# Kernel tuning notes

Measured on AMD Instinct MI355X. Metric: run time of the kernel, lower is better.

The kernel has to match this reference:

```python
import jax, jax.numpy as jnp
import numpy as np
import math

D_MODEL = 256
PRED_LEN = 256
K = 32
LOW_FREQ = 1


def setup_inputs() -> dict:
    key = jax.random.key(0)
    x = jax.random.normal(key, (8, 1024, D_MODEL), dtype=jnp.float32)
    return {"x": x}


def reference(x):
    """x: (b, t, d) -> reconstructed/extrapolated series (b, t+pred_len, d)."""
    b, t, d = x.shape
    k_ = K  # K < t//2, so the explicit-k branch of the torch module is taken

    x_freq = jnp.fft.rfft(x, axis=1)  # (b, t//2+1, d) complex
    if t % 2 == 0:
        x_freq_high = x_freq[:, LOW_FREQ:-1]  # drop DC..low_freq-1 and Nyquist
    else:
        x_freq_high = x_freq[:, LOW_FREQ:]

    # top-k magnitudes over the frequency axis, independently per (b, d)
    mag = jnp.abs(x_freq_high)                                   # (b, F, d)
    _, idx = jax.lax.top_k(jnp.transpose(mag, (0, 2, 1)), k_)    # (b, d, k)
    idx = jnp.transpose(idx, (0, 2, 1)) + LOW_FREQ               # (b, k, d) into x_freq

    x_freq_topk = jnp.take_along_axis(x_freq, idx, axis=1)       # (b, k, d) complex
    freqs = jnp.fft.rfftfreq(t).astype(x.dtype)                  # (t//2+1,)
    f_topk = freqs[idx]                                          # (b, k, d)

    # append conjugate / negative-frequency pair for a real reconstruction
    x_ext = jnp.concatenate([x_freq_topk, jnp.conj(x_freq_topk)], axis=1)  # (b, 2k, d)
    f_ext = jnp.concatenate([f_topk, -f_topk], axis=1)                     # (b, 2k, d)

    t_val = jnp.arange(t + PRED_LEN, dtype=x.dtype)              # (T,)
    amp = (jnp.abs(x_ext) / t)[:, :, None, :]                    # (b, 2k, 1, d)
    phase = jnp.angle(x_ext)[:, :, None, :]                      # (b, 2k, 1, d)
    arg = (2.0 * math.pi) * f_ext[:, :, None, :] * t_val[None, None, :, None] + phase
    x_time = amp * jnp.cos(arg)                                  # (b, 2k, T, d)
    return jnp.sum(x_time, axis=1)                               # (b, T, d)
```

## Files before the change

kernel.cpp:

```cpp
#include <hip/hip_runtime.h>
#include <math.h>

#define T_LEN 1024
#define PRED_LEN 256
#define OUT_T (T_LEN + PRED_LEN)
#define DM 256
#define KSEL 32
#define RTAU 1e-4f

#define PAD16(i) ((i) + ((i) >> 4))
#define C1024F 0.006135923151542565f

__device__ __constant__ float W16RF[16] = {
    1.0f,  0.92387953f,  0.70710678f,  0.38268343f, 0.0f, -0.38268343f, -0.70710678f, -0.92387953f,
   -1.0f, -0.92387953f, -0.70710678f, -0.38268343f, 0.0f,  0.38268343f,  0.70710678f,  0.92387953f };
__device__ __constant__ float W16IF[16] = {
    0.0f, -0.38268343f, -0.70710678f, -0.92387953f, -1.0f, -0.92387953f, -0.70710678f, -0.38268343f,
    0.0f,  0.38268343f,  0.70710678f,  0.92387953f,  1.0f,  0.92387953f,  0.70710678f,  0.38268343f };

#define C1_ 0.92387953251128675613
#define C2_ 0.70710678118654752440
#define C3_ 0.38268343236508977173
__device__ __constant__ double W16R_[16] = {
    1.0,  C1_,  C2_,  C3_, 0.0, -C3_, -C2_, -C1_,
   -1.0, -C1_, -C2_, -C3_, 0.0,  C3_,  C2_,  C1_ };
__device__ __constant__ double W16I_[16] = {
    0.0, -C3_, -C2_, -C1_, -1.0, -C1_, -C2_, -C3_,
    0.0,  C3_,  C2_,  C1_,  1.0,  C1_,  C2_,  C3_ };

__device__ __forceinline__ float2 zval(const float2* __restrict__ xunp,
                                       const unsigned* __restrict__ selw, int k) {
    if (k == 0 || k == 512) return float2{ 0.f, 0.f };
    const int  fold = (k < 512) ? k : (1024 - k);
    const float sgn = (k < 512) ? 1.0f : -1.0f;
    float2 X0 = xunp[fold];
    float2 X1 = xunp[512 + fold];
    const bool s0 = (selw[fold >> 5]        >> (fold & 31)) & 1u;
    const bool s1 = (selw[16 + (fold >> 5)] >> (fold & 31)) & 1u;
    float x0i = sgn * X0.y;
    float x1i = sgn * X1.y;
    float Zr = (s0 ? X0.x : 0.f) - (s1 ? x1i : 0.f);
    float Zi = (s0 ? x0i : 0.f) + (s1 ? X1.x : 0.f);
    return float2{ Zr, -Zi };
}

__device__ __forceinline__ void fft1024(const float2* __restrict__ xin,
                                        const float2* __restrict__ twF,
                                        int lane, int w, float* ar, float* ai) {
    float Fr[4][4], Fi[4][4];
#pragma unroll
    for (int n1a = 0; n1a < 4; ++n1a) {
        float2 a  = xin[lane + 64 * (n1a + 0)];
        float2 bb = xin[lane + 64 * (n1a + 4)];
        float2 cV = xin[lane + 64 * (n1a + 8)];
        float2 d  = xin[lane + 64 * (n1a + 12)];
        float t0r = a.x + cV.x, t0i = a.y + cV.y;
        float t1r = a.x - cV.x, t1i = a.y - cV.y;
        float t2r = bb.x + d.x, t2i = bb.y + d.y;
        float t3r = bb.x - d.x, t3i = bb.y - d.y;
        Fr[n1a][0] = t0r + t2r;  Fi[n1a][0] = t0i + t2i;
        Fr[n1a][2] = t0r - t2r;  Fi[n1a][2] = t0i - t2i;
        Fr[n1a][1] = t1r + t3i;  Fi[n1a][1] = t1i - t3r;
        Fr[n1a][3] = t1r - t3i;  Fi[n1a][3] = t1i + t3r;
    }
#pragma unroll
    for (int q = 0; q < 4; ++q) {
        const int k1 = (w << 2) | q;
        float cr = Fr[0][q], ci = Fi[0][q];
#pragma unroll
        for (int n1a = 1; n1a < 4; ++n1a) {
            int e = (n1a * k1) & 15;
            float wr = W16RF[e], wi = W16IF[e];
            cr += Fr[n1a][q] * wr - Fi[n1a][q] * wi;
            ci += Fr[n1a][q] * wi + Fi[n1a][q] * wr;
        }
        float2 tw = twF[PAD16((lane * k1) & 1023)];
        ar[q] = cr * tw.x - ci * tw.y;
        ai[q] = cr * tw.y + ci * tw.x;
    }
#pragma unroll
    for (int s = 0; s < 6; ++s) {
        const int half = 32 >> s;
        const int e = (lane & (half - 1)) << s;
        float2 tw = twF[PAD16(e << 4)];
        const bool up = (lane & half) != 0;
#pragma unroll
        for (int q = 0; q < 4; ++q) {
            float orr = __shfl_xor(ar[q], half);
            float oii = __shfl_xor(ai[q], half);
            float sr = ar[q] + orr, si = ai[q] + oii;
            float dr = orr - ar[q], di = oii - ai[q];
            ar[q] = up ? (dr * tw.x - di * tw.y) : sr;
            ai[q] = up ? (dr * tw.y + di * tw.x) : si;
        }
    }
}

__device__ __forceinline__ void fft1024_z(const float2* __restrict__ xunp,
                                          const unsigned* __restrict__ selw,
                                          const float2* __restrict__ twF,
                                          int lane, int w, float* ar, float* ai) {
    float Fr[4][4], Fi[4][4];
#pragma unroll
    for (int n1a = 0; n1a < 4; ++n1a) {
        float2 a  = zval(xunp, selw, lane + 64 * (n1a + 0));
        float2 bb = zval(xunp, selw, lane + 64 * (n1a + 4));
        float2 cV = zval(xunp, selw, lane + 64 * (n1a + 8));
        float2 d  = zval(xunp, selw, lane + 64 * (n1a + 12));
        float t0r = a.x + cV.x, t0i = a.y + cV.y;
        float t1r = a.x - cV.x, t1i = a.y - cV.y;
        float t2r = bb.x + d.x, t2i = bb.y + d.y;
        float t3r = bb.x - d.x, t3i = bb.y - d.y;
        Fr[n1a][0] = t0r + t2r;  Fi[n1a][0] = t0i + t2i;
        Fr[n1a][2] = t0r - t2r;  Fi[n1a][2] = t0i - t2i;
        Fr[n1a][1] = t1r + t3i;  Fi[n1a][1] = t1i - t3r;
        Fr[n1a][3] = t1r - t3i;  Fi[n1a][3] = t1i + t3r;
    }
#pragma unroll
    for (int q = 0; q < 4; ++q) {
        const int k1 = (w << 2) | q;
        float cr = Fr[0][q], ci = Fi[0][q];
#pragma unroll
        for (int n1a = 1; n1a < 4; ++n1a) {
            int e = (n1a * k1) & 15;
            float wr = W16RF[e], wi = W16IF[e];
            cr += Fr[n1a][q] * wr - Fi[n1a][q] * wi;
            ci += Fr[n1a][q] * wi + Fi[n1a][q] * wr;
        }
        float2 tw = twF[PAD16((lane * k1) & 1023)];
        ar[q] = cr * tw.x - ci * tw.y;
        ai[q] = cr * tw.y + ci * tw.x;
    }
#pragma unroll
    for (int s = 0; s < 6; ++s) {
        const int half = 32 >> s;
        const int e = (lane & (half - 1)) << s;
        float2 tw = twF[PAD16(e << 4)];
        const bool up = (lane & half) != 0;
#pragma unroll
        for (int q = 0; q < 4; ++q) {
            float orr = __shfl_xor(ar[q], half);
            float oii = __shfl_xor(ai[q], half);
            float sr = ar[q] + orr, si = ai[q] + oii;
            float dr = orr - ar[q], di = oii - ai[q];
            ar[q] = up ? (dr * tw.x - di * tw.y) : sr;
            ai[q] = up ? (dr * tw.y + di * tw.x) : si;
        }
    }
}

__global__ void __launch_bounds__(256, 4)
fl_fused_kernel(const float* __restrict__ x, float* __restrict__ out) {
    __shared__ float2 twF[PAD16(1023) + 1];
    __shared__ float2 spP[PAD16(1023) + 1];
    __shared__ char smemU[8192];
    __shared__ int hist[512];
    __shared__ unsigned selw[32];
    float2* xsh  = (float2*)smemU;
    float2* xunp = (float2*)smemU;

    const int tid  = threadIdx.x;
    const int lane = tid & 63;
    const int w    = tid >> 6;

    const int bid = blockIdx.x;
    const int sp  = ((bid & 7) << 7) | (bid >> 3);
    const int b   = sp >> 7;
    const int d0  = (sp & 127) << 1;

    for (int j = 0; j < 4; ++j) {
        int e = tid + (j << 8);
        float sn, cs;
        __sincosf((float)e * C1024F, &sn, &cs);
        twF[PAD16(e)] = float2{ cs, -sn };
        xsh[e] = *reinterpret_cast<const float2*>(&x[(((size_t)(b << 10) + e) << 8) + d0]);
    }
    if (tid < 32) selw[tid] = 0u;
    __syncthreads();

    float ar[4], ai[4];
    fft1024(xsh, twF, lane, w, ar, ai);

    const int krev = (int)(__brev((unsigned)lane) >> 26);
#pragma unroll
    for (int q = 0; q < 4; ++q) {
        int k = ((w << 2) | q) + (krev << 4);
        spP[PAD16(k)] = float2{ ar[q], ai[q] };
    }
    __syncthreads();

    if (tid < 128) {
        const int c = tid >> 6;
        int* histc = hist + (c << 8);

        float v[8]; int hiw[8];
#pragma unroll
        for (int q = 0; q < 8; ++q) {
            int m = (q << 6) | lane;
            int n = (1024 - m) & 1023;
            float2 Pk = spP[PAD16(m)];
            float2 Pn = spP[PAD16(n)];
            float rr, ii;
            if (c == 0) { rr = 0.5f * (Pk.x + Pn.x); ii = 0.5f * (Pk.y - Pn.y); }
            else        { rr = 0.5f * (Pk.y + Pn.y); ii = 0.5f * (Pn.x - Pk.x); }
            v[q] = rr * rr + ii * ii;
        }
        if (lane == 0) v[0] = -1.0f;
#pragma unroll
        for (int q = 0; q < 8; ++q) hiw[q] = __float_as_int(v[q]);

        int mx = hiw[0];
#pragma unroll
        for (int q = 1; q < 8; ++q) mx = max(mx, hiw[q]);
#pragma unroll
        for (int off = 1; off < 64; off <<= 1) mx = max(mx, __shfl_xor(mx, off));

        const int base = (mx >> 20) - 250;
        int idx[8];
#pragma unroll
        for (int q = 0; q < 8; ++q) {
            int t = (hiw[q] >> 20) - base;
            idx[q] = t < 0 ? 0 : t;
        }

        *reinterpret_cast<int4*>(&histc[lane << 2]) = int4{0, 0, 0, 0};
#pragma unroll
        for (int q = 0; q < 8; ++q) atomicAdd(&histc[idx[q]], 1);

        int4 cc = *reinterpret_cast<int4*>(&histc[lane << 2]);
        int s_local = cc.x + cc.y + cc.z + cc.w;

        int s = s_local;
#pragma unroll
        for (int off = 1; off < 64; off <<= 1) {
            int t = __shfl_down(s, off);
            if (lane + off < 64) s += t;
        }
        const int S_gt = s - s_local;
        const int A3 = S_gt;
        const int A2 = A3 + cc.w;
        const int A1 = A2 + cc.z;
        const int A0 = A1 + cc.y;

        int foundB = -1, foundR = 0;
        if (A0 < KSEL && A0 + cc.x >= KSEL) { foundB = (lane << 2) | 0; foundR = KSEL - A0; }
        if (A1 < KSEL && A1 + cc.y >= KSEL) { foundB = (lane << 2) | 1; foundR = KSEL - A1; }
        if (A2 < KSEL && A2 + cc.z >= KSEL) { foundB = (lane << 2) | 2; foundR = KSEL - A2; }
        if (A3 < KSEL && A3 + cc.w >= KSEL) { foundB = (lane << 2) | 3; foundR = KSEL - A3; }

        unsigned long long fm = __ballot(foundB >= 0);
        const int srcB = (int)(__ffsll((unsigned long long)fm) - 1);
        int B = __shfl(foundB, srcB);
        int r = __shfl(foundR, srcB);

        unsigned selmask = 0, candmask = 0;
#pragma unroll
        for (int q = 0; q < 8; ++q) {
            if (idx[q] > B) selmask |= (1u << q);
            else if (idx[q] == B) candmask |= (1u << q);
        }

        if (r > 0 && B > 0) {
            *reinterpret_cast<int4*>(&histc[lane << 2]) = int4{0, 0, 0, 0};
            int idx2[8];
#pragma unroll
            for (int q = 0; q < 8; ++q) {
                idx2[q] = (hiw[q] >> 12) & 255;
                if ((candmask >> q) & 1u) atomicAdd(&histc[idx2[q]], 1);
            }
            int4 c2 = *reinterpret_cast<int4*>(&histc[lane << 2]);
            int s2l = c2.x + c2.y + c2.z + c2.w;
            int ss = s2l;
#pragma unroll
            for (int off = 1; off < 64; off <<= 1) {
                int t = __shfl_down(ss, off);
                if (lane + off < 64) ss += t;
            }
            const int G3 = ss - s2l;
            const int G2 = G3 + c2.w;
            const int G1 = G2 + c2.z;
            const int G0 = G1 + c2.y;
            int fB2 = -1, fR2 = 0;
            if (G0 < r && G0 + c2.x >= r) { fB2 = (lane << 2) | 0; fR2 = r - G0; }
            if (G1 < r && G1 + c2.y >= r) { fB2 = (lane << 2) | 1; fR2 = r - G1; }
            if (G2 < r && G2 + c2.z >= r) { fB2 = (lane << 2) | 2; fR2 = r - G2; }
            if (G3 < r && G3 + c2.w >= r) { fB2 = (lane << 2) | 3; fR2 = r - G3; }
            unsigned long long fm2 = __ballot(fB2 >= 0);
            const int src2 = (int)(__ffsll((unsigned long long)fm2) - 1);
            const int Bb = __shfl(fB2, src2);
            const int rr = __shfl(fR2, src2);
            unsigned newcand = 0;
#pragma unroll
            for (int q = 0; q < 8; ++q) {
                if ((candmask >> q) & 1u) {
                    if (idx2[q] > Bb) selmask |= (1u << q);
                    else if (idx2[q] == Bb) newcand |= (1u << q);
                }
            }
            candmask = newcand;
            r = rr;
        }

        for (int it = 0; it < r; ++it) {
            float bv = -2.0f; int bq = -1;
#pragma unroll
            for (int q = 0; q < 8; ++q) {
                bool cand = ((candmask >> q) & 1u) != 0;
                if (cand && v[q] > bv) { bv = v[q]; bq = q; }
            }
            int bi = (bq < 0) ? 0x7FFFFFFF : ((bq << 6) | lane);
#pragma unroll
            for (int off = 1; off < 64; off <<= 1) {
                float ov = __shfl_xor(bv, off);
                int   oi = __shfl_xor(bi, off);
                if (ov > bv || (ov == bv && oi < bi)) { bv = ov; bi = oi; }
            }
            if (bi != 0x7FFFFFFF && lane == (bi & 63)) {
                unsigned bit = 1u << (bi >> 6);
                selmask  |= bit;
                candmask &= ~bit;
            }
        }

        {
            float vminS = 3.0e38f, vmaxU = -3.0e38f;
#pragma unroll
            for (int q = 0; q < 8; ++q) {
                if ((selmask >> q) & 1u) vminS = fminf(vminS, v[q]);
                else                     vmaxU = fmaxf(vmaxU, v[q]);
            }
#pragma unroll
            for (int off = 1; off < 64; off <<= 1) {
                vminS = fminf(vminS, __shfl_xor(vminS, off));
                vmaxU = fmaxf(vmaxU, __shfl_xor(vmaxU, off));
            }
            const float tau = RTAU * vminS;
            if (vminS - vmaxU < tau) {
                const float lo = vmaxU - tau, hi = vminS + tau;
                unsigned candq = 0; int nAbove = 0;
#pragma unroll
                for (int q = 0; q < 8; ++q) {
                    bool inw = (v[q] >= lo) && (v[q] <= hi);
                    if (inw) candq |= (1u << q);
                    if (((selmask >> q) & 1u) && v[q] > hi) ++nAbove;
                }
#pragma unroll
                for (int off = 1; off < 64; off <<= 1) nAbove += __shfl_xor(nAbove, off);
                const int kneed = KSEL - nAbove;
                selmask &= ~candq;

                const float* xcol = x + ((size_t)(b << 10) << 8) + d0 + c;
                double sV = -1.0; int sSrc = 0; int cnum = 0;
                for (int q = 0; q < 8; ++q) {
                    unsigned long long bal = __ballot((candq >> q) & 1u);
                    while (bal) {
                        int srcl = (int)(__ffsll(bal) - 1);
                        bal &= bal - 1;
                        int m = (q << 6) | srcl;
                        double th0 = (double)((m * lane) & 1023)
                                   * (-6.283185307179586476925286766559 / 1024.0);
                        double wr, wi;
                        { double s0, c0; sincos(th0, &s0, &c0); wr = c0; wi = s0; }
                        const double stR = W16R_[m & 15], stI = W16I_[m & 15];
                        double sr = 0.0, si = 0.0;
#pragma unroll
                        for (int u = 0; u < 16; ++u) {
                            int n = lane + (u << 6);
                            double xvd = (double)xcol[(size_t)n << 8];
                            sr = fma(xvd, wr, sr);
                            si = fma(xvd, wi, si);
                            double nwr = wr * stR - wi * stI;
                            double nwi = wr * stI + wi * stR;
                            wr = nwr; wi = nwi;
                        }
#pragma unroll
                        for (int off = 1; off < 64; off <<= 1) {
                            sr += __shfl_xor(sr, off);
                            si += __shfl_xor(si, off);
                        }
                        if (lane == cnum) { sV = sr * sr + si * si; sSrc = (q << 6) | srcl; }
                        ++cnum;
                        if (cnum >= 64) break;
                    }
                    if (cnum >= 64) break;
                }
                for (int it = 0; it < kneed; ++it) {
                    double bv = sV; int bl = lane;
#pragma unroll
                    for (int off = 1; off < 64; off <<= 1) {
                        double ov = __shfl_xor(bv, off);
                        int    ol = __shfl_xor(bl, off);
                        if (ov > bv || (ov == bv && ol < bl)) { bv = ov; bl = ol; }
                    }
                    int wsrc = __shfl(sSrc, bl);
                    if (lane == (wsrc & 63)) selmask |= 1u << (wsrc >> 6);
                    if (lane == bl) sV = -2.0;
                }
            }
        }

#pragma unroll
        for (int q = 0; q < 8; ++q) {
            if ((selmask >> q) & 1u) {
                int m = (q << 6) | lane;
                atomicOr(&selw[(c << 4) | (m >> 5)], 1u << (m & 31));
            }
        }
    } else {
        const int t2 = tid - 128;
#pragma unroll
        for (int j = 0; j < 4; ++j) {
            int k = t2 + (j << 7);
            int n = (1024 - k) & 1023;
            float2 Pk = spP[PAD16(k)];
            float2 Pn = spP[PAD16(n)];
            xunp[k]       = float2{ 0.5f * (Pk.x + Pn.x), 0.5f * (Pk.y - Pn.y) };
            xunp[512 + k] = float2{ 0.5f * (Pk.y + Pn.y), 0.5f * (Pn.x - Pk.x) };
        }
    }
    __syncthreads();

    fft1024_z(xunp, selw, twF, lane, w, ar, ai);

    {
        const float S = 1.0f / 1024.0f;
        float2* o2 = reinterpret_cast<float2*>(out + (size_t)b * OUT_T * DM + d0);
#pragma unroll
        for (int q = 0; q < 4; ++q) {
            int t = ((w << 2) | q) + (krev << 4);
            float2 o{ ar[q] * S, -ai[q] * S };
            o2[(size_t)t * 128] = o;
            if (t < PRED_LEN) o2[(size_t)(t + T_LEN) * 128] = o;
        }
    }
}

extern "C" void kernel_launch(void* const* d_in, const int* in_sizes, int n_in,
                              void* d_out, int out_size, void* d_ws, size_t ws_size,
                              hipStream_t stream) {
    const float* x = (const float*)d_in[0];
    float* out = (float*)d_out;
    hipLaunchKernelGGL(fl_fused_kernel, dim3(1024), dim3(256), 0, stream, x, out);
}
```

Baseline: 35.36 us.

## Replace paired-column 1024-point FFT with per-column half-length real FFT

```diff
diff --git a/kernel.cpp b/kernel.cpp
--- a/kernel.cpp
+++ b/kernel.cpp
@@ -8,15 +8,13 @@
 #define KSEL 32
 #define RTAU 1e-4f
 
-#define PAD16(i) ((i) + ((i) >> 4))
+#define PADH(i) ((i) + ((i) >> 4))
+#define C512F  0.012271846303085130f
 #define C1024F 0.006135923151542565f
 
-__device__ __constant__ float W16RF[16] = {
-    1.0f,  0.92387953f,  0.70710678f,  0.38268343f, 0.0f, -0.38268343f, -0.70710678f, -0.92387953f,
-   -1.0f, -0.92387953f, -0.70710678f, -0.38268343f, 0.0f,  0.38268343f,  0.70710678f,  0.92387953f };
-__device__ __constant__ float W16IF[16] = {
-    0.0f, -0.38268343f, -0.70710678f, -0.92387953f, -1.0f, -0.92387953f, -0.70710678f, -0.38268343f,
-    0.0f,  0.38268343f,  0.70710678f,  0.92387953f,  1.0f,  0.92387953f,  0.70710678f,  0.38268343f };
+#define R2F 0.70710678118654752440f
+__device__ __constant__ float W8RF[8] = { 1.f,  R2F, 0.f, -R2F, -1.f, -R2F, 0.f,  R2F };
+__device__ __constant__ float W8IF[8] = { 0.f, -R2F, -1.f, -R2F, 0.f,  R2F, 1.f,  R2F };
 
 #define C1_ 0.92387953251128675613
 #define C2_ 0.70710678118654752440
@@ -28,53 +26,42 @@
     0.0, -C3_, -C2_, -C1_, -1.0, -C1_, -C2_, -C3_,
     0.0,  C3_,  C2_,  C1_,  1.0,  C1_,  C2_,  C3_ };
 
-__device__ __forceinline__ float2 zval(const float2* __restrict__ xunp,
-                                       const unsigned* __restrict__ selw, int k) {
-    if (k == 0 || k == 512) return float2{ 0.f, 0.f };
-    const int  fold = (k < 512) ? k : (1024 - k);
-    const float sgn = (k < 512) ? 1.0f : -1.0f;
-    float2 X0 = xunp[fold];
-    float2 X1 = xunp[512 + fold];
-    const bool s0 = (selw[fold >> 5]        >> (fold & 31)) & 1u;
-    const bool s1 = (selw[16 + (fold >> 5)] >> (fold & 31)) & 1u;
-    float x0i = sgn * X0.y;
-    float x1i = sgn * X1.y;
-    float Zr = (s0 ? X0.x : 0.f) - (s1 ? x1i : 0.f);
-    float Zi = (s0 ? x0i : 0.f) + (s1 ? X1.x : 0.f);
-    return float2{ Zr, -Zi };
+__device__ __forceinline__ float2 gval(const float2* __restrict__ xt,
+                                       const unsigned* __restrict__ selw,
+                                       const float2* __restrict__ twH, int k) {
+    if (k == 0) return float2{ 0.f, 0.f };
+    const int kk = 512 - k;
+    const bool sk  = (selw[k  >> 5] >> (k  & 31)) & 1u;
+    const bool skk = (selw[kk >> 5] >> (kk & 31)) & 1u;
+    float2 Yk = xt[PADH(k)];  if (!sk)  Yk = float2{ 0.f, 0.f };
+    float2 Ym = xt[PADH(kk)]; if (!skk) Ym = float2{ 0.f, 0.f };
+    float Epr = 0.5f * (Yk.x + Ym.x), Epi = 0.5f * (Yk.y - Ym.y);
+    float Dpr = 0.5f * (Yk.x - Ym.x), Dpi = 0.5f * (Yk.y + Ym.y);
+    float2 twc = twH[PADH(k)];
+    float wr = twc.x, wi = -twc.y;
+    float Opr = Dpr * wr - Dpi * wi;
+    float Opi = Dpr * wi + Dpi * wr;
+    return float2{ Epr - Opi, -(Epi + Opr) };
 }
 
-__device__ __forceinline__ void fft1024(const float2* __restrict__ xin,
-                                        const float2* __restrict__ twF,
-                                        int lane, int w, float* ar, float* ai) {
-    float Fr[4][4], Fi[4][4];
-#pragma unroll
-    for (int n1a = 0; n1a < 4; ++n1a) {
-        float2 a  = xin[lane + 64 * (n1a + 0)];
-        float2 bb = xin[lane + 64 * (n1a + 4)];
-        float2 cV = xin[lane + 64 * (n1a + 8)];
-        float2 d  = xin[lane + 64 * (n1a + 12)];
-        float t0r = a.x + cV.x, t0i = a.y + cV.y;
-        float t1r = a.x - cV.x, t1i = a.y - cV.y;
-        float t2r = bb.x + d.x, t2i = bb.y + d.y;
-        float t3r = bb.x - d.x, t3i = bb.y - d.y;
-        Fr[n1a][0] = t0r + t2r;  Fi[n1a][0] = t0i + t2i;
-        Fr[n1a][2] = t0r - t2r;  Fi[n1a][2] = t0i - t2i;
-        Fr[n1a][1] = t1r + t3i;  Fi[n1a][1] = t1i - t3r;
-        Fr[n1a][3] = t1r - t3i;  Fi[n1a][3] = t1i + t3r;
-    }
-#pragma unroll
-    for (int q = 0; q < 4; ++q) {
-        const int k1 = (w << 2) | q;
-        float cr = Fr[0][q], ci = Fi[0][q];
-#pragma unroll
-        for (int n1a = 1; n1a < 4; ++n1a) {
-            int e = (n1a * k1) & 15;
-            float wr = W16RF[e], wi = W16IF[e];
-            cr += Fr[n1a][q] * wr - Fi[n1a][q] * wi;
-            ci += Fr[n1a][q] * wi + Fi[n1a][q] * wr;
-        }
-        float2 tw = twF[PAD16((lane * k1) & 1023)];
+__device__ __forceinline__ void fft512(const float2* __restrict__ zin,
+                                       const float2* __restrict__ tw512,
+                                       int lane, int w, float* ar, float* ai) {
+    float2 zv[8];
+#pragma unroll
+    for (int n1 = 0; n1 < 8; ++n1) zv[n1] = zin[PADH(lane + (n1 << 6))];
+#pragma unroll
+    for (int q = 0; q < 2; ++q) {
+        const int k1 = (w << 1) | q;
+        float cr = 0.f, ci = 0.f;
+#pragma unroll
+        for (int n1 = 0; n1 < 8; ++n1) {
+            int e = (k1 * n1) & 7;
+            float wr = W8RF[e], wi = W8IF[e];
+            cr += zv[n1].x * wr - zv[n1].y * wi;
+            ci += zv[n1].x * wi + zv[n1].y * wr;
+        }
+        float2 tw = tw512[PADH(lane * k1)];
         ar[q] = cr * tw.x - ci * tw.y;
         ai[q] = cr * tw.y + ci * tw.x;
     }
@@ -82,10 +69,10 @@
     for (int s = 0; s < 6; ++s) {
         const int half = 32 >> s;
         const int e = (lane & (half - 1)) << s;
-        float2 tw = twF[PAD16(e << 4)];
+        float2 tw = tw512[PADH(e << 3)];
         const bool up = (lane & half) != 0;
 #pragma unroll
-        for (int q = 0; q < 4; ++q) {
+        for (int q = 0; q < 2; ++q) {
             float orr = __shfl_xor(ar[q], half);
             float oii = __shfl_xor(ai[q], half);
             float sr = ar[q] + orr, si = ai[q] + oii;
@@ -96,38 +83,26 @@
     }
 }
 
-__device__ __forceinline__ void fft1024_z(const float2* __restrict__ xunp,
-                                          const unsigned* __restrict__ selw,
-                                          const float2* __restrict__ twF,
-                                          int lane, int w, float* ar, float* ai) {
-    float Fr[4][4], Fi[4][4];
-#pragma unroll
-    for (int n1a = 0; n1a < 4; ++n1a) {
-        float2 a  = zval(xunp, selw, lane + 64 * (n1a + 0));
-        float2 bb = zval(xunp, selw, lane + 64 * (n1a + 4));
-        float2 cV = zval(xunp, selw, lane + 64 * (n1a + 8));
-        float2 d  = zval(xunp, selw, lane + 64 * (n1a + 12));
-        float t0r = a.x + cV.x, t0i = a.y + cV.y;
-        float t1r = a.x - cV.x, t1i = a.y - cV.y;
-        float t2r = bb.x + d.x, t2i = bb.y + d.y;
-        float t3r = bb.x - d.x, t3i = bb.y - d.y;
-        Fr[n1a][0] = t0r + t2r;  Fi[n1a][0] = t0i + t2i;
-        Fr[n1a][2] = t0r - t2r;  Fi[n1a][2] = t0i - t2i;
-        Fr[n1a][1] = t1r + t3i;  Fi[n1a][1] = t1i - t3r;
-        Fr[n1a][3] = t1r - t3i;  Fi[n1a][3] = t1i + t3r;
-    }
-#pragma unroll
-    for (int q = 0; q < 4; ++q) {
-        const int k1 = (w << 2) | q;
-        float cr = Fr[0][q], ci = Fi[0][q];
-#pragma unroll
-        for (int n1a = 1; n1a < 4; ++n1a) {
-            int e = (n1a * k1) & 15;
-            float wr = W16RF[e], wi = W16IF[e];
-            cr += Fr[n1a][q] * wr - Fi[n1a][q] * wi;
-            ci += Fr[n1a][q] * wi + Fi[n1a][q] * wr;
-        }
-        float2 tw = twF[PAD16((lane * k1) & 1023)];
+__device__ __forceinline__ void fft512_g(const float2* __restrict__ xt,
+                                         const unsigned* __restrict__ selw,
+                                         const float2* __restrict__ twH,
+                                         const float2* __restrict__ tw512,
+                                         int lane, int w, float* ar, float* ai) {
+    float2 zv[8];
+#pragma unroll
+    for (int n1 = 0; n1 < 8; ++n1) zv[n1] = gval(xt, selw, twH, lane + (n1 << 6));
+#pragma unroll
+    for (int q = 0; q < 2; ++q) {
+        const int k1 = (w << 1) | q;
+        float cr = 0.f, ci = 0.f;
+#pragma unroll
+        for (int n1 = 0; n1 < 8; ++n1) {
+            int e = (k1 * n1) & 7;
+            float wr = W8RF[e], wi = W8IF[e];
+            cr += zv[n1].x * wr - zv[n1].y * wi;
+            ci += zv[n1].x * wi + zv[n1].y * wr;
+        }
+        float2 tw = tw512[PADH(lane * k1)];
         ar[q] = cr * tw.x - ci * tw.y;
         ai[q] = cr * tw.y + ci * tw.x;
     }
@@ -135,10 +110,10 @@
     for (int s = 0; s < 6; ++s) {
         const int half = 32 >> s;
         const int e = (lane & (half - 1)) << s;
-        float2 tw = twF[PAD16(e << 4)];
+        float2 tw = tw512[PADH(e << 3)];
         const bool up = (lane & half) != 0;
 #pragma unroll
-        for (int q = 0; q < 4; ++q) {
+        for (int q = 0; q < 2; ++q) {
             float orr = __shfl_xor(ar[q], half);
             float oii = __shfl_xor(ai[q], half);
             float sr = ar[q] + orr, si = ai[q] + oii;
@@ -149,61 +124,68 @@
     }
 }
 
-__global__ void __launch_bounds__(256, 4)
+__global__ void __launch_bounds__(256)
 fl_fused_kernel(const float* __restrict__ x, float* __restrict__ out) {
-    __shared__ float2 twF[PAD16(1023) + 1];
-    __shared__ float2 spP[PAD16(1023) + 1];
-    __shared__ char smemU[8192];
-    __shared__ int hist[512];
-    __shared__ unsigned selw[32];
-    float2* xsh  = (float2*)smemU;
-    float2* xunp = (float2*)smemU;
+    __shared__ float2 tw512[PADH(511) + 1];
+    __shared__ float2 twH[PADH(511) + 1];
+    __shared__ float2 arrA[PADH(511) + 1];
+    __shared__ float2 arrB[PADH(511) + 1];
+    __shared__ int hist[256];
+    __shared__ unsigned selw[16];
 
     const int tid  = threadIdx.x;
     const int lane = tid & 63;
     const int w    = tid >> 6;
 
     const int bid = blockIdx.x;
-    const int sp  = ((bid & 7) << 7) | (bid >> 3);
-    const int b   = sp >> 7;
-    const int d0  = (sp & 127) << 1;
-
-    for (int j = 0; j < 4; ++j) {
+    const int b   = bid & 7;
+    const int d   = bid >> 3;
+
+    for (int j = 0; j < 2; ++j) {
         int e = tid + (j << 8);
         float sn, cs;
+        __sincosf((float)e * C512F, &sn, &cs);
+        tw512[PADH(e)] = float2{ cs, -sn };
         __sincosf((float)e * C1024F, &sn, &cs);
-        twF[PAD16(e)] = float2{ cs, -sn };
-        xsh[e] = *reinterpret_cast<const float2*>(&x[(((size_t)(b << 10) + e) << 8) + d0]);
-    }
-    if (tid < 32) selw[tid] = 0u;
+        twH[PADH(e)] = float2{ cs, -sn };
+    }
+    {
+        const float* xc = x + (((size_t)b << 10) << 8) + d;
+        float* zf = (float*)arrA;
+        for (int j = 0; j < 4; ++j) {
+            int t = tid + (j << 8);
+            float xv = xc[(size_t)t << 8];
+            zf[2 * PADH(t >> 1) + (t & 1)] = xv;
+        }
+    }
+    if (tid < 16) selw[tid] = 0u;
     __syncthreads();
 
-    float ar[4], ai[4];
-    fft1024(xsh, twF, lane, w, ar, ai);
-
+    float ar[2], ai[2];
+    fft512(arrA, tw512, lane, w, ar, ai);
     const int krev = (int)(__brev((unsigned)lane) >> 26);
 #pragma unroll
-    for (int q = 0; q < 4; ++q) {
-        int k = ((w << 2) | q) + (krev << 4);
-        spP[PAD16(k)] = float2{ ar[q], ai[q] };
+    for (int q = 0; q < 2; ++q) {
+        int k = ((w << 1) | q) + (krev << 3);
+        arrB[PADH(k)] = float2{ ar[q], ai[q] };
     }
     __syncthreads();
 
-    if (tid < 128) {
-        const int c = tid >> 6;
-        int* histc = hist + (c << 8);
-
+    if (tid < 64) {
         float v[8]; int hiw[8];
 #pragma unroll
         for (int q = 0; q < 8; ++q) {
             int m = (q << 6) | lane;
-            int n = (1024 - m) & 1023;
-            float2 Pk = spP[PAD16(m)];
-            float2 Pn = spP[PAD16(n)];
-            float rr, ii;
-            if (c == 0) { rr = 0.5f * (Pk.x + Pn.x); ii = 0.5f * (Pk.y - Pn.y); }
-            else        { rr = 0.5f * (Pk.y + Pn.y); ii = 0.5f * (Pn.x - Pk.x); }
-            v[q] = rr * rr + ii * ii;
+            int n = (512 - m) & 511;
+            float2 Zk = arrB[PADH(m & 511)];
+            float2 Zm = arrB[PADH(n)];
+            float Er = 0.5f * (Zk.x + Zm.x), Ei = 0.5f * (Zk.y - Zm.y);
+            float Dr = 0.5f * (Zk.x - Zm.x), Di = 0.5f * (Zk.y + Zm.y);
+            float Or = Di, Oi = -Dr;
+            float2 tw = twH[PADH(m)];
+            float Xr = Er + Or * tw.x - Oi * tw.y;
+            float Xi = Ei + Or * tw.y + Oi * tw.x;
+            v[q] = Xr * Xr + Xi * Xi;
         }
         if (lane == 0) v[0] = -1.0f;
 #pragma unroll
@@ -223,11 +205,11 @@
             idx[q] = t < 0 ? 0 : t;
         }
 
-        *reinterpret_cast<int4*>(&histc[lane << 2]) = int4{0, 0, 0, 0};
-#pragma unroll
-        for (int q = 0; q < 8; ++q) atomicAdd(&histc[idx[q]], 1);
-
-        int4 cc = *reinterpret_cast<int4*>(&histc[lane << 2]);
+        *reinterpret_cast<int4*>(&hist[lane << 2]) = int4{0, 0, 0, 0};
+#pragma unroll
+        for (int q = 0; q < 8; ++q) atomicAdd(&hist[idx[q]], 1);
+
+        int4 cc = *reinterpret_cast<int4*>(&hist[lane << 2]);
         int s_local = cc.x + cc.y + cc.z + cc.w;
 
         int s = s_local;
@@ -261,14 +243,14 @@
         }
 
         if (r > 0 && B > 0) {
-            *reinterpret_cast<int4*>(&histc[lane << 2]) = int4{0, 0, 0, 0};
+            *reinterpret_cast<int4*>(&hist[lane << 2]) = int4{0, 0, 0, 0};
             int idx2[8];
 #pragma unroll
             for (int q = 0; q < 8; ++q) {
                 idx2[q] = (hiw[q] >> 12) & 255;
-                if ((candmask >> q) & 1u) atomicAdd(&histc[idx2[q]], 1);
-            }
-            int4 c2 = *reinterpret_cast<int4*>(&histc[lane << 2]);
+                if ((candmask >> q) & 1u) atomicAdd(&hist[idx2[q]], 1);
+            }
+            int4 c2 = *reinterpret_cast<int4*>(&hist[lane << 2]);
             int s2l = c2.x + c2.y + c2.z + c2.w;
             int ss = s2l;
 #pragma unroll
@@ -349,7 +331,7 @@
                 const int kneed = KSEL - nAbove;
                 selmask &= ~candq;
 
-                const float* xcol = x + ((size_t)(b << 10) << 8) + d0 + c;
+                const float* xcol = x + (((size_t)b << 10) << 8) + d;
                 double sV = -1.0; int sSrc = 0; int cnum = 0;
                 for (int q = 0; q < 8; ++q) {
                     unsigned long long bal = __ballot((candq >> q) & 1u);
@@ -403,34 +385,43 @@
         for (int q = 0; q < 8; ++q) {
             if ((selmask >> q) & 1u) {
                 int m = (q << 6) | lane;
-                atomicOr(&selw[(c << 4) | (m >> 5)], 1u << (m & 31));
-            }
-        }
-    } else {
-        const int t2 = tid - 128;
+                atomicOr(&selw[m >> 5], 1u << (m & 31));
+            }
+        }
+    } else if (tid < 192) {
+        const int t2 = tid - 64;
 #pragma unroll
         for (int j = 0; j < 4; ++j) {
             int k = t2 + (j << 7);
-            int n = (1024 - k) & 1023;
-            float2 Pk = spP[PAD16(k)];
-            float2 Pn = spP[PAD16(n)];
-            xunp[k]       = float2{ 0.5f * (Pk.x + Pn.x), 0.5f * (Pk.y - Pn.y) };
-            xunp[512 + k] = float2{ 0.5f * (Pk.y + Pn.y), 0.5f * (Pn.x - Pk.x) };
+            int n = (512 - k) & 511;
+            float2 Zk = arrB[PADH(k)];
+            float2 Zm = arrB[PADH(n)];
+            float Er = 0.5f * (Zk.x + Zm.x), Ei = 0.5f * (Zk.y - Zm.y);
+            float Dr = 0.5f * (Zk.x - Zm.x), Di = 0.5f * (Zk.y + Zm.y);
+            float Or = Di, Oi = -Dr;
+            float2 tw = twH[PADH(k)];
+            arrA[PADH(k)] = float2{ Er + Or * tw.x - Oi * tw.y,
+                                    Ei + Or * tw.y + Oi * tw.x };
         }
     }
     __syncthreads();
 
-    fft1024_z(xunp, selw, twF, lane, w, ar, ai);
+    fft512_g(arrA, selw, twH, tw512, lane, w, ar, ai);
 
     {
-        const float S = 1.0f / 1024.0f;
-        float2* o2 = reinterpret_cast<float2*>(out + (size_t)b * OUT_T * DM + d0);
-#pragma unroll
-        for (int q = 0; q < 4; ++q) {
-            int t = ((w << 2) | q) + (krev << 4);
-            float2 o{ ar[q] * S, -ai[q] * S };
-            o2[(size_t)t * 128] = o;
-            if (t < PRED_LEN) o2[(size_t)(t + T_LEN) * 128] = o;
+        const float S = 1.0f / 512.0f;
+        float* ob = out + ((size_t)b * OUT_T) * DM + d;
+#pragma unroll
+        for (int q = 0; q < 2; ++q) {
+            int n = ((w << 1) | q) + (krev << 3);
+            float y0 = ar[q] * S;
+            float y1 = -ai[q] * S;
+            ob[(size_t)(2 * n)     << 8] = y0;
+            ob[(size_t)(2 * n + 1) << 8] = y1;
+            if (n < 128) {
+                ob[(size_t)(2 * n + T_LEN)     << 8] = y0;
+                ob[(size_t)(2 * n + 1 + T_LEN) << 8] = y1;
+            }
         }
     }
 }
@@ -440,5 +431,5 @@
                               hipStream_t stream) {
     const float* x = (const float*)d_in[0];
     float* out = (float*)d_out;
-    hipLaunchKernelGGL(fl_fused_kernel, dim3(1024), dim3(256), 0, stream, x, out);
+    hipLaunchKernelGGL(fl_fused_kernel, dim3(2048), dim3(256), 0, stream, x, out);
 }
```

Result: slower. 50.68 us (+43.3%).
